# Kernel optimization log

Hardware: AMD Instinct MI355X
Metric: run time of the kernel (lower is better)

## Reference

```python
import jax, jax.numpy as jnp
import numpy as np

EMBED = 1024
HEADS = 8
HEAD_DIM = EMBED // HEADS
WINDOW = 128
B, T = 2, 2048


def setup_inputs() -> dict:
    key = jax.random.key(0)
    ks = jax.random.split(key, 6)
    s_in = 1.0 / np.sqrt(EMBED)
    return {
        "x": jax.random.normal(ks[0], (B, T, EMBED), dtype=jnp.float32),
        "W_qkv": jax.random.normal(ks[1], (EMBED, 3 * EMBED), dtype=jnp.float32) * s_in,
        "b_qkv": jax.random.normal(ks[2], (3 * EMBED,), dtype=jnp.float32) * 0.01,
        "W_proj": jax.random.normal(ks[3], (EMBED, EMBED), dtype=jnp.float32) * s_in,
        "b_proj": jax.random.normal(ks[4], (EMBED,), dtype=jnp.float32) * 0.01,
        "gate": jnp.ones((EMBED,), dtype=jnp.float32),
    }


def reference(x, W_qkv, b_qkv, W_proj, b_proj, gate):
    Bb, Tt, C = x.shape
    qkv = x @ W_qkv + b_qkv                       # [B,T,3C]
    q, k, v = jnp.split(qkv, 3, axis=-1)
    # [B,H,T,D]
    q = q.reshape(Bb, Tt, HEADS, HEAD_DIM).transpose(0, 2, 1, 3)
    k = k.reshape(Bb, Tt, HEADS, HEAD_DIM).transpose(0, 2, 1, 3)
    v = v.reshape(Bb, Tt, HEADS, HEAD_DIM).transpose(0, 2, 1, 3)
    scale = 1.0 / np.sqrt(HEAD_DIM).astype(np.float32)
    att = jnp.einsum('bhqd,bhkd->bhqk', q, k) * scale
    idx = jnp.arange(Tt)
    # causal AND within |i-j| <= window  (diagonal always valid -> no all-masked rows)
    mask = (idx[:, None] >= idx[None, :]) & (jnp.abs(idx[:, None] - idx[None, :]) <= WINDOW)
    att = jnp.where(mask[None, None], att, -jnp.inf)
    att = jax.nn.softmax(att, axis=-1)
    out = jnp.einsum('bhqk,bhkd->bhqd', att, v)
    out = out.transpose(0, 2, 1, 3).reshape(Bb, Tt, C)
    return (out * gate) @ W_proj + b_proj
```

## Files before the change

kernel.cpp:

```cpp
#include <hip/hip_runtime.h>

typedef unsigned short u16;
typedef unsigned int u32;
typedef __attribute__((ext_vector_type(4))) float f32x4;
typedef __attribute__((ext_vector_type(8))) short bf16x8;
typedef __attribute__((ext_vector_type(8))) unsigned short u16x8;

#define SEQ   2048
#define NB    2
#define NH    8
#define HD    128
#define EMB   1024
#define WIN   128
#define MTOT  4096
#define NQKV  3072
#define HSZ   (SEQ*HD)
#define QKVSZ (NB*NH*HSZ)

static __device__ __forceinline__ u16 f2bf(float f){
  u32 x = __builtin_bit_cast(u32, f);
  x += 0x7fffu + ((x >> 16) & 1u);
  return (u16)(x >> 16);
}

static __device__ __forceinline__ void gload_lds16(const void* g, void* l){
  __builtin_amdgcn_global_load_lds((__attribute__((address_space(1))) void*)(void*)(g),
                                   (__attribute__((address_space(3))) void*)(l), 16, 0, 0);
}


__global__ __launch_bounds__(256) void prep(
    const float* __restrict__ x, const float* __restrict__ Wqkv,
    const float* __restrict__ Wproj,
    u16* __restrict__ Xb, u16* __restrict__ Wqt, u16* __restrict__ Wpt)
{
  __shared__ float tile[32][33];
  const int b = blockIdx.x, tid = threadIdx.x;
  if (b < 2048){
    const int i = (b * 256 + tid) * 8;
    float4 a = *(const float4*)(x + i);
    float4 c = *(const float4*)(x + i + 4);
    uint4 o;
    o.x = (u32)f2bf(a.x) | ((u32)f2bf(a.y) << 16);
    o.y = (u32)f2bf(a.z) | ((u32)f2bf(a.w) << 16);
    o.z = (u32)f2bf(c.x) | ((u32)f2bf(c.y) << 16);
    o.w = (u32)f2bf(c.z) | ((u32)f2bf(c.w) << 16);
    *(uint4*)(Xb + i) = o;
    return;
  }
  const float* in; u16* out; int R, C, bxi, byi;
  if (b < 5120){
    const int bb = b - 2048;
    in = Wqkv; out = Wqt; R = EMB; C = NQKV;
    bxi = bb % 96; byi = bb / 96;
  } else {
    const int bb = b - 5120;
    in = Wproj; out = Wpt; R = EMB; C = EMB;
    bxi = bb & 31; byi = bb >> 5;
  }
  const int bx = bxi * 32, by = byi * 32;
  const int tx = tid & 31, ty = tid >> 5;
  #pragma unroll
  for (int i = 0; i < 32; i += 8)
    tile[ty + i][tx] = in[(size_t)(by + ty + i) * C + bx + tx];
  __syncthreads();
  #pragma unroll
  for (int i = 0; i < 32; i += 8)
    out[(size_t)(bx + ty + i) * R + by + tx] = f2bf(tile[tx][ty + i]);
}


__global__ __launch_bounds__(256) void gemm_qkv(
    const u16* __restrict__ A,
    const u16* __restrict__ Bt,
    const float* __restrict__ bias,
    u16* __restrict__ obf)
{
  constexpr int K = 1024, BK = 64;
  __shared__ u16 As[128 * 64];
  __shared__ u16 Bs[128 * 64];
  const int tid = threadIdx.x, lane = tid & 63, wave = tid >> 6;
  const int m0 = blockIdx.y * 128, n0 = blockIdx.x * 128;
  const int wr = (wave >> 1) * 64, wc = (wave & 1) * 64;

  const int srow = lane >> 3;
  const int scol = ((((lane & 7) << 4) ^ (srow << 4)) >> 1);
  const u16* ag = A  + (size_t)(m0 + wave * 32 + srow) * K + scol;
  const u16* bg = Bt + (size_t)(n0 + wave * 32 + srow) * K + scol;
  u16* al = &As[wave * 32 * 64];
  u16* bl = &Bs[wave * 32 * 64];

  f32x4 acc[4][4] = {};

  for (int kt = 0; kt < K / BK; ++kt){
    #pragma unroll
    for (int j = 0; j < 4; ++j){
      gload_lds16(ag + (size_t)j * 8 * K + kt * BK, al + j * 8 * 64);
      gload_lds16(bg + (size_t)j * 8 * K + kt * BK, bl + j * 8 * 64);
    }
    __syncthreads();
    #pragma unroll
    for (int ks = 0; ks < 2; ++ks){
      const int fr = lane & 15;
      const int colb = ((ks << 6) + ((lane >> 4) << 4)) ^ ((lane & 7) << 4);
      bf16x8 af[4], bfr[4];
      #pragma unroll
      for (int mi = 0; mi < 4; ++mi)
        af[mi] = *(const bf16x8*)((const char*)As + (wr + mi * 16 + fr) * 128 + colb);
      #pragma unroll
      for (int ni = 0; ni < 4; ++ni)
        bfr[ni] = *(const bf16x8*)((const char*)Bs + (wc + ni * 16 + fr) * 128 + colb);
      #pragma unroll
      for (int mi = 0; mi < 4; ++mi)
        #pragma unroll
        for (int ni = 0; ni < 4; ++ni)
          acc[mi][ni] = __builtin_amdgcn_mfma_f32_16x16x32_bf16(af[mi], bfr[ni], acc[mi][ni], 0, 0, 0);
    }
    __syncthreads();
  }

  #pragma unroll
  for (int mi = 0; mi < 4; ++mi){
    const int rg = m0 + wr + mi * 16 + ((lane >> 4) << 2);
    const int b_ = rg >> 11, t = rg & 2047;
    #pragma unroll
    for (int ni = 0; ni < 4; ++ni){
      const int cg = n0 + wc + ni * 16 + (lane & 15);
      const float bs = bias[cg];
      const int which = cg >> 10, hm = cg & 1023;
      u16* dst = obf + (size_t)which * QKVSZ
                     + ((size_t)(b_ * NH + (hm >> 7)) * SEQ + t) * HD + (hm & 127);
      #pragma unroll
      for (int j = 0; j < 4; ++j)
        dst[(size_t)j * HD] = f2bf(acc[mi][ni][j] + bs);
    }
  }
}


__global__ __launch_bounds__(256) void gemm_proj(
    const u16* __restrict__ A,
    const u16* __restrict__ Bt,
    const float* __restrict__ bias,
    float* __restrict__ of)
{
  constexpr int K = 1024, BK = 64;
  __shared__ u16 As[128 * 64];
  __shared__ u16 Bs[64 * 64];
  const int tid = threadIdx.x, lane = tid & 63, wave = tid >> 6;
  const int m0 = blockIdx.y * 128, n0 = blockIdx.x * 64;
  const int wr = (wave >> 1) * 64, wc = (wave & 1) * 32;
  const int fr = lane & 15, hk = lane >> 4;

  const int prow = tid >> 3;
  const int sw8 = (tid & 7) ^ (prow & 7);
  const u16* ag = A  + (size_t)(m0 + prow) * K + sw8 * 8;
  const u16* bg = Bt + (size_t)(n0 + prow) * K + sw8 * 8;

  f32x4 acc[4][2] = {};

  for (int kt = 0; kt < K / BK; ++kt){
    #pragma unroll
    for (int r = 0; r < 4; ++r)
      gload_lds16(ag + (size_t)(r * 32) * K + kt * BK, (char*)As + r * 4096 + tid * 16);
    #pragma unroll
    for (int r = 0; r < 2; ++r)
      gload_lds16(bg + (size_t)(r * 32) * K + kt * BK, (char*)Bs + r * 4096 + tid * 16);
    __syncthreads();
    #pragma unroll
    for (int ks = 0; ks < 2; ++ks){
      bf16x8 af[4], bfr[2];
      #pragma unroll
      for (int mi = 0; mi < 4; ++mi){
        const int r = wr + mi * 16 + fr;
        const int cb = ((ks << 6) + (hk << 4)) ^ ((r & 7) << 4);
        af[mi] = *(const bf16x8*)((const char*)As + r * 128 + cb);
      }
      #pragma unroll
      for (int ni = 0; ni < 2; ++ni){
        const int r = wc + ni * 16 + fr;
        const int cb = ((ks << 6) + (hk << 4)) ^ ((r & 7) << 4);
        bfr[ni] = *(const bf16x8*)((const char*)Bs + r * 128 + cb);
      }
      #pragma unroll
      for (int mi = 0; mi < 4; ++mi)
        #pragma unroll
        for (int ni = 0; ni < 2; ++ni)
          acc[mi][ni] = __builtin_amdgcn_mfma_f32_16x16x32_bf16(af[mi], bfr[ni], acc[mi][ni], 0, 0, 0);
    }
    __syncthreads();
  }

  #pragma unroll
  for (int mi = 0; mi < 4; ++mi){
    const int rg = m0 + wr + mi * 16 + (hk << 2);
    #pragma unroll
    for (int ni = 0; ni < 2; ++ni){
      const int cg = n0 + wc + ni * 16 + fr;
      const float bs = bias[cg];
      #pragma unroll
      for (int j = 0; j < 4; ++j)
        of[(size_t)(rg + j) * EMB + cg] = acc[mi][ni][j] + bs;
    }
  }
}


__global__ __launch_bounds__(256) void attn_kernel(
    const u16* __restrict__ QKVb, const float* __restrict__ gate, u16* __restrict__ Ao)
{
  __shared__ float S[64 * 196];
  __shared__ u16 KV[128 * 72];
  const int tid = threadIdx.x, lane = tid & 63, wave = tid >> 6;
  const int q0 = blockIdx.x * 64;
  const int bh = blockIdx.y;
  const u16* Qg = QKVb + (size_t)bh * HSZ;
  const u16* Kg = QKVb + (size_t)QKVSZ + (size_t)bh * HSZ;
  const u16* Vg = QKVb + (size_t)2 * QKVSZ + (size_t)bh * HSZ;
  const int kstart = q0 - WIN;

  bf16x8 qf[4];
  {
    const u16* qp = Qg + (size_t)(q0 + wave * 16 + (lane & 15)) * HD + 8 * (lane >> 4);
    #pragma unroll
    for (int ks = 0; ks < 4; ++ks) qf[ks] = *(const bf16x8*)(qp + ks * 32);
  }
  const float scale = 0.08838834764831845f;

  for (int c = 0; c < 3; ++c){
    if (kstart + c * 64 + 64 <= 0){
      for (int t2 = tid; t2 < 64 * 64; t2 += 256)
        S[(t2 >> 6) * 196 + c * 64 + (t2 & 63)] = -1e30f;
      continue;
    }
    {
      const int keyl = tid >> 2;
      int krow = kstart + c * 64 + keyl;
      krow = min(max(krow, 0), SEQ - 1);
      const u16* kp = Kg + (size_t)krow * HD + (tid & 3) * 8;
      u16* ksh = &KV[keyl * 136 + (tid & 3) * 8];
      #pragma unroll
      for (int r = 0; r < 4; ++r)
        *(uint4*)(ksh + r * 32) = *(const uint4*)(kp + r * 32);
    }
    __syncthreads();
    f32x4 sacc[4] = {};
    #pragma unroll
    for (int ks = 0; ks < 4; ++ks){
      #pragma unroll
      for (int nf = 0; nf < 4; ++nf){
        bf16x8 kf = *(const bf16x8*)(&KV[(nf * 16 + (lane & 15)) * 136 + ks * 32 + 8 * (lane >> 4)]);
        sacc[nf] = __builtin_amdgcn_mfma_f32_16x16x32_bf16(qf[ks], kf, sacc[nf], 0, 0, 0);
      }
    }
    #pragma unroll
    for (int nf = 0; nf < 4; ++nf){
      const int kc = c * 64 + nf * 16 + (lane & 15);
      const int kg = kstart + kc;
      #pragma unroll
      for (int j = 0; j < 4; ++j){
        const int qr = wave * 16 + ((lane >> 4) << 2) + j;
        const int qg = q0 + qr;
        const bool ok = (kg >= 0) && (kg <= qg) && (qg - kg <= WIN);
        S[qr * 196 + kc] = ok ? sacc[nf][j] * scale : -1e30f;
      }
    }
    __syncthreads();
  }

  {
    const int r = tid >> 2, sub = tid & 3;
    float4 v[12];
    float mx = -1e30f;
    #pragma unroll
    for (int i = 0; i < 12; ++i){
      v[i] = *(const float4*)(&S[r * 196 + (sub + 4 * i) * 4]);
      mx = fmaxf(mx, fmaxf(fmaxf(v[i].x, v[i].y), fmaxf(v[i].z, v[i].w)));
    }
    mx = fmaxf(mx, __shfl_xor(mx, 1));
    mx = fmaxf(mx, __shfl_xor(mx, 2));
    float sum = 0.f;
    #pragma unroll
    for (int i = 0; i < 12; ++i){
      v[i].x = __expf(v[i].x - mx); v[i].y = __expf(v[i].y - mx);
      v[i].z = __expf(v[i].z - mx); v[i].w = __expf(v[i].w - mx);
      sum += v[i].x + v[i].y + v[i].z + v[i].w;
    }
    sum += __shfl_xor(sum, 1);
    sum += __shfl_xor(sum, 2);
    const float inv = 1.0f / sum;
    #pragma unroll
    for (int i = 0; i < 12; ++i){
      v[i].x *= inv; v[i].y *= inv; v[i].z *= inv; v[i].w *= inv;
      *(float4*)(&S[r * 196 + (sub + 4 * i) * 4]) = v[i];
    }
  }
  __syncthreads();

  f32x4 oacc[8] = {};
  for (int c = 0; c < 3; ++c){
    if (kstart + c * 64 + 64 <= 0) continue;
    {
      const int keyl = tid & 63;
      int krow = kstart + c * 64 + keyl;
      krow = min(max(krow, 0), SEQ - 1);
      const u16* vp = Vg + (size_t)krow * HD + (tid >> 6) * 32;
      #pragma unroll
      for (int r2 = 0; r2 < 4; ++r2){
        u16x8 vv = *(const u16x8*)(vp + r2 * 8);
        const int dbase = (tid >> 6) * 32 + r2 * 8;
        #pragma unroll
        for (int j = 0; j < 8; ++j)
          KV[(dbase + j) * 72 + keyl] = vv[j];
      }
    }
    __syncthreads();
    #pragma unroll
    for (int ks = 0; ks < 2; ++ks){
      const float* sp = &S[(wave * 16 + (lane & 15)) * 196 + c * 64 + ks * 32 + 8 * (lane >> 4)];
      float4 p0 = *(const float4*)sp;
      float4 p1 = *(const float4*)(sp + 4);
      bf16x8 pf;
      pf[0] = (short)f2bf(p0.x); pf[1] = (short)f2bf(p0.y);
      pf[2] = (short)f2bf(p0.z); pf[3] = (short)f2bf(p0.w);
      pf[4] = (short)f2bf(p1.x); pf[5] = (short)f2bf(p1.y);
      pf[6] = (short)f2bf(p1.z); pf[7] = (short)f2bf(p1.w);
      #pragma unroll
      for (int nf = 0; nf < 8; ++nf){
        bf16x8 vf = *(const bf16x8*)(&KV[(nf * 16 + (lane & 15)) * 72 + ks * 32 + 8 * (lane >> 4)]);
        oacc[nf] = __builtin_amdgcn_mfma_f32_16x16x32_bf16(pf, vf, oacc[nf], 0, 0, 0);
      }
    }
    __syncthreads();
  }

  {
    const int b = bh >> 3, h = bh & 7;
    #pragma unroll
    for (int nf = 0; nf < 8; ++nf){
      const int d = nf * 16 + (lane & 15);
      const float gv = gate[h * HD + d];
      #pragma unroll
      for (int j = 0; j < 4; ++j){
        const int t = q0 + wave * 16 + ((lane >> 4) << 2) + j;
        Ao[((size_t)(b * SEQ + t)) * EMB + h * HD + d] = f2bf(oacc[nf][j] * gv);
      }
    }
  }
}


extern "C" void kernel_launch(void* const* d_in, const int* in_sizes, int n_in,
                              void* d_out, int out_size, void* d_ws, size_t ws_size,
                              hipStream_t stream)
{
  const float* x     = (const float*)d_in[0];
  const float* Wqkv  = (const float*)d_in[1];
  const float* bqkv  = (const float*)d_in[2];
  const float* Wproj = (const float*)d_in[3];
  const float* bproj = (const float*)d_in[4];
  const float* gate  = (const float*)d_in[5];
  float* out = (float*)d_out;

  u16* Xb   = (u16*)d_ws;
  u16* Wqt  = Xb   + (size_t)MTOT * EMB;
  u16* Wpt  = Wqt  + (size_t)NQKV * EMB;
  u16* QKVb = Wpt  + (size_t)EMB * EMB;
  u16* Ao   = QKVb + (size_t)3 * QKVSZ;

  prep<<<dim3(6144), dim3(256), 0, stream>>>(x, Wqkv, Wproj, Xb, Wqt, Wpt);

  gemm_qkv<<<dim3(NQKV / 128, MTOT / 128), dim3(256), 0, stream>>>(Xb, Wqt, bqkv, QKVb);

  attn_kernel<<<dim3(SEQ / 64, NB * NH), dim3(256), 0, stream>>>(QKVb, gate, Ao);

  gemm_proj<<<dim3(EMB / 64, MTOT / 128), dim3(256), 0, stream>>>(Ao, Wpt, bproj, out);
}
```

Measured before the change: 148.1 us.

## Stage GEMM and attention epilogues through LDS for vectorized coalesced stores

All three kernels now write their output tiles into shared memory first, then store them to global memory as 16-byte vectors in row-contiguous order, instead of scattered 2- or 4-byte stores. The QKV GEMM also switches to a 1D grid with a block-index swizzle that groups neighbouring tiles per XCD for better L2 reuse. The cost is an extra LDS round trip and a barrier in each epilogue, and the shared buffers are reused so the staging must not overlap live data.

After: 161.6 us. 1.09x slower.

```diff
diff --git a/kernel.cpp b/kernel.cpp
--- a/kernel.cpp
+++ b/kernel.cpp
@@ -77,11 +77,17 @@
     u16* __restrict__ obf)
 {
   constexpr int K = 1024, BK = 64;
-  __shared__ u16 As[128 * 64];
-  __shared__ u16 Bs[128 * 64];
+  __shared__ char smem[128 * 132 * 2];
+  u16* As = (u16*)smem;
+  u16* Bs = (u16*)(smem + 16384);
+  u16* Ct = (u16*)smem;
+
   const int tid = threadIdx.x, lane = tid & 63, wave = tid >> 6;
-  const int m0 = blockIdx.y * 128, n0 = blockIdx.x * 128;
+  const int bid = blockIdx.x;
+  const int swz = (bid & 7) * 96 + (bid >> 3);
+  const int m0 = (swz / 24) * 128, n0 = (swz % 24) * 128;
   const int wr = (wave >> 1) * 64, wc = (wave & 1) * 64;
+  const int fr = lane & 15, hk = lane >> 4;
 
   const int srow = lane >> 3;
   const int scol = ((((lane & 7) << 4) ^ (srow << 4)) >> 1);
@@ -101,8 +107,7 @@
     __syncthreads();
     #pragma unroll
     for (int ks = 0; ks < 2; ++ks){
-      const int fr = lane & 15;
-      const int colb = ((ks << 6) + ((lane >> 4) << 4)) ^ ((lane & 7) << 4);
+      const int colb = ((ks << 6) + (hk << 4)) ^ ((lane & 7) << 4);
       bf16x8 af[4], bfr[4];
       #pragma unroll
       for (int mi = 0; mi < 4; ++mi)
@@ -121,19 +126,27 @@
 
   #pragma unroll
   for (int mi = 0; mi < 4; ++mi){
-    const int rg = m0 + wr + mi * 16 + ((lane >> 4) << 2);
+    const int r = wr + mi * 16 + (hk << 2);
+    #pragma unroll
+    for (int ni = 0; ni < 4; ++ni){
+      const int c = wc + ni * 16 + fr;
+      const float bs = bias[n0 + c];
+      #pragma unroll
+      for (int j = 0; j < 4; ++j)
+        Ct[(r + j) * 132 + c] = f2bf(acc[mi][ni][j] + bs);
+    }
+  }
+  __syncthreads();
+  #pragma unroll
+  for (int it = 0; it < 8; ++it){
+    const int flat = it * 256 + tid;
+    const int row = flat >> 4, col8 = (flat & 15) * 8;
+    u16x8 v = *(const u16x8*)(Ct + row * 132 + col8);
+    const int rg = m0 + row, cg = n0 + col8;
     const int b_ = rg >> 11, t = rg & 2047;
-    #pragma unroll
-    for (int ni = 0; ni < 4; ++ni){
-      const int cg = n0 + wc + ni * 16 + (lane & 15);
-      const float bs = bias[cg];
-      const int which = cg >> 10, hm = cg & 1023;
-      u16* dst = obf + (size_t)which * QKVSZ
-                     + ((size_t)(b_ * NH + (hm >> 7)) * SEQ + t) * HD + (hm & 127);
-      #pragma unroll
-      for (int j = 0; j < 4; ++j)
-        dst[(size_t)j * HD] = f2bf(acc[mi][ni][j] + bs);
-    }
+    const int which = cg >> 10, hm = cg & 1023;
+    *(u16x8*)(obf + (size_t)which * QKVSZ
+                  + ((size_t)(b_ * NH + (hm >> 7)) * SEQ + t) * HD + (hm & 127)) = v;
   }
 }
 
@@ -145,8 +158,11 @@
     float* __restrict__ of)
 {
   constexpr int K = 1024, BK = 64;
-  __shared__ u16 As[128 * 64];
-  __shared__ u16 Bs[64 * 64];
+  __shared__ char smem[128 * 72 * 4];
+  u16* As = (u16*)smem;
+  u16* Bs = (u16*)(smem + 16384);
+  float* Ct = (float*)smem;
+
   const int tid = threadIdx.x, lane = tid & 63, wave = tid >> 6;
   const int m0 = blockIdx.y * 128, n0 = blockIdx.x * 64;
   const int wr = (wave >> 1) * 64, wc = (wave & 1) * 32;
@@ -193,15 +209,23 @@
 
   #pragma unroll
   for (int mi = 0; mi < 4; ++mi){
-    const int rg = m0 + wr + mi * 16 + (hk << 2);
+    const int r = wr + mi * 16 + (hk << 2);
     #pragma unroll
     for (int ni = 0; ni < 2; ++ni){
-      const int cg = n0 + wc + ni * 16 + fr;
-      const float bs = bias[cg];
+      const int c = wc + ni * 16 + fr;
+      const float bs = bias[n0 + c];
       #pragma unroll
       for (int j = 0; j < 4; ++j)
-        of[(size_t)(rg + j) * EMB + cg] = acc[mi][ni][j] + bs;
-    }
+        Ct[(r + j) * 72 + c] = acc[mi][ni][j] + bs;
+    }
+  }
+  __syncthreads();
+  #pragma unroll
+  for (int it = 0; it < 8; ++it){
+    const int flat = it * 256 + tid;
+    const int row = flat >> 4, col4 = (flat & 15) * 4;
+    float4 v = *(const float4*)(Ct + row * 72 + col4);
+    *(float4*)(of + (size_t)(m0 + row) * EMB + n0 + col4) = v;
   }
 }
 
@@ -335,16 +359,26 @@
   }
 
   {
+    u16* T2 = (u16*)S;
     const int b = bh >> 3, h = bh & 7;
+    const int fr_ = lane & 15, hk_ = lane >> 4;
     #pragma unroll
     for (int nf = 0; nf < 8; ++nf){
-      const int d = nf * 16 + (lane & 15);
+      const int d = nf * 16 + fr_;
       const float gv = gate[h * HD + d];
       #pragma unroll
       for (int j = 0; j < 4; ++j){
-        const int t = q0 + wave * 16 + ((lane >> 4) << 2) + j;
-        Ao[((size_t)(b * SEQ + t)) * EMB + h * HD + d] = f2bf(oacc[nf][j] * gv);
-      }
+        const int qr = wave * 16 + (hk_ << 2) + j;
+        T2[qr * 132 + d] = f2bf(oacc[nf][j] * gv);
+      }
+    }
+    __syncthreads();
+    #pragma unroll
+    for (int it = 0; it < 4; ++it){
+      const int flat = it * 256 + tid;
+      const int row = flat >> 4, col8 = (flat & 15) * 8;
+      u16x8 v = *(const u16x8*)(T2 + row * 132 + col8);
+      *(u16x8*)(Ao + ((size_t)(b * SEQ + q0 + row)) * EMB + h * HD + col8) = v;
     }
   }
 }
@@ -370,7 +404,7 @@
 
   prep<<<dim3(6144), dim3(256), 0, stream>>>(x, Wqkv, Wproj, Xb, Wqt, Wpt);
 
-  gemm_qkv<<<dim3(NQKV / 128, MTOT / 128), dim3(256), 0, stream>>>(Xb, Wqt, bqkv, QKVb);
+  gemm_qkv<<<dim3(768), dim3(256), 0, stream>>>(Xb, Wqt, bqkv, QKVb);
 
   attn_kernel<<<dim3(SEQ / 64, NB * NH), dim3(256), 0, stream>>>(QKVb, gate, Ao);
 
```
